# Kernel tuning notes

Hardware: AMD Instinct MI355X
Metric: run time of the kernel (lower is better)

## Reference

```python
import jax, jax.numpy as jnp
import numpy as np

B, TQ, TK, H = 8, 64, 8192, 256


def setup_inputs() -> dict:
    key = jax.random.key(0)
    k1, k2, k3, k4 = jax.random.split(key, 4)
    query = jax.random.normal(k1, (B, TQ, H), dtype=jnp.float32)
    keys = jax.random.normal(k2, (B, TK, H), dtype=jnp.float32)
    # nn.Linear(H, H): weight [H, H], bias [H]; scale like torch default-ish
    Wa_w = jax.random.normal(k3, (H, H), dtype=jnp.float32) * (1.0 / np.sqrt(H))
    Wa_b = jax.random.normal(k4, (H,), dtype=jnp.float32) * 0.01
    return {"query": query, "keys": keys, "Wa_w": Wa_w, "Wa_b": Wa_b}


def reference(query, keys, Wa_w, Wa_b):
    # keys_transformed = keys @ Wa_w.T + Wa_b  (torch Linear semantics)
    keys_t = jnp.einsum('bkh,oh->bko', keys, Wa_w) + Wa_b  # [B,TK,H]
    scores = jnp.einsum('bqh,bkh->bqk', query, keys_t)       # [B,TQ,TK]
    weights = jax.nn.softmax(scores, axis=-1)
    context = jnp.einsum('bqk,bkh->bqh', weights, keys)      # [B,TQ,H]
    return (context, weights)
```

## Files before the change

kernel.cpp:

```cpp
#include <hip/hip_runtime.h>

#define B 8
#define TQ 64
#define TK 8192
#define H 256

#define SPADB 72

#define KSPLIT 32
#define KPB (TK / KSPLIT)
#define CH 64
#define CKC 64
#define CPAD 68

typedef __attribute__((ext_vector_type(8))) short bf16x8;
typedef __attribute__((ext_vector_type(4))) float f32x4;
typedef __attribute__((ext_vector_type(4))) unsigned short u16x4;

static __device__ inline unsigned short f2bf(float x) {
    unsigned int u = __float_as_uint(x);
    unsigned int r = (u + 0x7fffu + ((u >> 16) & 1u)) >> 16;
    return (unsigned short)r;
}
static __device__ inline float bf2f(unsigned short h) {
    return __uint_as_float(((unsigned int)h) << 16);
}

__global__ __launch_bounds__(256) void qtransform_kernel(
    const float* __restrict__ query, const float* __restrict__ Wa_w,
    const float* __restrict__ Wa_b, float* __restrict__ qt, float* __restrict__ qb)
{
    __shared__ float q_s[H];
    __shared__ float red[4];
    const int r = blockIdx.x;
    const int t = threadIdx.x;
    q_s[t] = query[r * H + t];
    __syncthreads();

    float a0 = 0.f, a1 = 0.f, a2 = 0.f, a3 = 0.f;
    for (int o = 0; o < H; o += 4) {
        a0 += q_s[o + 0] * Wa_w[(o + 0) * H + t];
        a1 += q_s[o + 1] * Wa_w[(o + 1) * H + t];
        a2 += q_s[o + 2] * Wa_w[(o + 2) * H + t];
        a3 += q_s[o + 3] * Wa_w[(o + 3) * H + t];
    }
    qt[r * H + t] = (a0 + a1) + (a2 + a3);

    float p = q_s[t] * Wa_b[t];
    for (int off = 32; off > 0; off >>= 1) p += __shfl_down(p, off, 64);
    if ((t & 63) == 0) red[t >> 6] = p;
    __syncthreads();
    if (t == 0) qb[r] = (red[0] + red[1]) + (red[2] + red[3]);
}

__global__ __launch_bounds__(256) void scores_kernel(
    const float* __restrict__ qt, const float* __restrict__ qb,
    const float* __restrict__ keys, float* __restrict__ wout)
{
    __shared__ unsigned short a_hi[TQ][SPADB], a_lo[TQ][SPADB];
    __shared__ unsigned short b_hi[64][SPADB], b_lo[64][SPADB];
    const int t    = threadIdx.x;
    const int kt   = blockIdx.x;
    const int b    = blockIdx.y;
    const int k0g  = kt * 64;
    const int w    = t >> 6;
    const int lane = t & 63;
    const int lrow = lane & 15;
    const int lgrp = lane >> 4;

    f32x4 acc[4];
    #pragma unroll
    for (int nt = 0; nt < 4; ++nt) acc[nt] = (f32x4){0.f, 0.f, 0.f, 0.f};

    for (int hc = 0; hc < H; hc += 64) {
        __syncthreads();
        #pragma unroll
        for (int i = 0; i < 4; ++i) {
            int idx = t + 256 * i;
            int row = idx >> 4, hf = idx & 15;
            float4 va = *(const float4*)&qt[(b * TQ + row) * H + hc + hf * 4];
            u16x4 h4, l4;
            h4[0] = f2bf(va.x); l4[0] = f2bf(va.x - bf2f(h4[0]));
            h4[1] = f2bf(va.y); l4[1] = f2bf(va.y - bf2f(h4[1]));
            h4[2] = f2bf(va.z); l4[2] = f2bf(va.z - bf2f(h4[2]));
            h4[3] = f2bf(va.w); l4[3] = f2bf(va.w - bf2f(h4[3]));
            *(u16x4*)&a_hi[row][hf * 4] = h4;
            *(u16x4*)&a_lo[row][hf * 4] = l4;

            float4 vb = *(const float4*)&keys[(size_t)(b * TK + k0g + row) * H + hc + hf * 4];
            u16x4 g4, m4;
            g4[0] = f2bf(vb.x); m4[0] = f2bf(vb.x - bf2f(g4[0]));
            g4[1] = f2bf(vb.y); m4[1] = f2bf(vb.y - bf2f(g4[1]));
            g4[2] = f2bf(vb.z); m4[2] = f2bf(vb.z - bf2f(g4[2]));
            g4[3] = f2bf(vb.w); m4[3] = f2bf(vb.w - bf2f(g4[3]));
            *(u16x4*)&b_hi[row][hf * 4] = g4;
            *(u16x4*)&b_lo[row][hf * 4] = m4;
        }
        __syncthreads();
        #pragma unroll
        for (int hs = 0; hs < 64; hs += 32) {
            bf16x8 ah = *(const bf16x8*)&a_hi[16 * w + lrow][hs + lgrp * 8];
            bf16x8 al = *(const bf16x8*)&a_lo[16 * w + lrow][hs + lgrp * 8];
            #pragma unroll
            for (int nt = 0; nt < 4; ++nt) {
                bf16x8 bh = *(const bf16x8*)&b_hi[16 * nt + lrow][hs + lgrp * 8];
                bf16x8 bl = *(const bf16x8*)&b_lo[16 * nt + lrow][hs + lgrp * 8];
                acc[nt] = __builtin_amdgcn_mfma_f32_16x16x32_bf16(ah, bh, acc[nt], 0, 0, 0);
                acc[nt] = __builtin_amdgcn_mfma_f32_16x16x32_bf16(ah, bl, acc[nt], 0, 0, 0);
                acc[nt] = __builtin_amdgcn_mfma_f32_16x16x32_bf16(al, bh, acc[nt], 0, 0, 0);
            }
        }
    }
    #pragma unroll
    for (int j = 0; j < 4; ++j) {
        const int qrow = 16 * w + lgrp * 4 + j;
        const float bias = qb[b * TQ + qrow];
        float* dst = &wout[(size_t)(b * TQ + qrow) * TK + k0g + lrow];
        #pragma unroll
        for (int nt = 0; nt < 4; ++nt) dst[16 * nt] = acc[nt][j] + bias;
    }
}

__global__ __launch_bounds__(1024) void softmax_kernel(float* __restrict__ w)
{
    const int r = blockIdx.x;
    const int t = threadIdx.x;
    float4* row4 = (float4*)(w + (size_t)r * TK);
    __shared__ float redm[16];
    __shared__ float reds[16];
    const int wid = t >> 6, lane = t & 63;

    float4 v0 = row4[t];
    float4 v1 = row4[t + 1024];
    float m = fmaxf(fmaxf(fmaxf(v0.x, v0.y), fmaxf(v0.z, v0.w)),
                    fmaxf(fmaxf(v1.x, v1.y), fmaxf(v1.z, v1.w)));
    for (int off = 32; off > 0; off >>= 1) m = fmaxf(m, __shfl_xor(m, off, 64));
    if (lane == 0) redm[wid] = m;
    __syncthreads();
    m = redm[0];
    #pragma unroll
    for (int i = 1; i < 16; ++i) m = fmaxf(m, redm[i]);

    v0.x = __expf(v0.x - m); v0.y = __expf(v0.y - m);
    v0.z = __expf(v0.z - m); v0.w = __expf(v0.w - m);
    v1.x = __expf(v1.x - m); v1.y = __expf(v1.y - m);
    v1.z = __expf(v1.z - m); v1.w = __expf(v1.w - m);
    float s = (v0.x + v0.y + v0.z + v0.w) + (v1.x + v1.y + v1.z + v1.w);
    for (int off = 32; off > 0; off >>= 1) s += __shfl_xor(s, off, 64);
    if (lane == 0) reds[wid] = s;
    __syncthreads();
    s = reds[0];
    #pragma unroll
    for (int i = 1; i < 16; ++i) s += reds[i];
    const float inv = 1.0f / s;

    v0.x *= inv; v0.y *= inv; v0.z *= inv; v0.w *= inv;
    v1.x *= inv; v1.y *= inv; v1.z *= inv; v1.w *= inv;
    row4[t] = v0;
    row4[t + 1024] = v1;
}

__global__ __launch_bounds__(256) void context_main_kernel(
    const float* __restrict__ w, const float* __restrict__ keys,
    float* __restrict__ part)
{
    __shared__ float w_s[TQ][CPAD];
    __shared__ float k_s[CKC][CPAD];
    const int t  = threadIdx.x;
    const int ks = blockIdx.x;
    const int ht = blockIdx.y;
    const int b  = blockIdx.z;
    const int tq = t >> 4, th = t & 15;
    const int q0 = tq * 4, h0 = th * 4;

    float acc[4][4];
    #pragma unroll
    for (int i = 0; i < 4; ++i)
        #pragma unroll
        for (int j = 0; j < 4; ++j) acc[i][j] = 0.f;

    for (int kc = 0; kc < KPB; kc += CKC) {
        const int k0 = ks * KPB + kc;
        __syncthreads();
        #pragma unroll
        for (int i = 0; i < 4; ++i) {
            int idx = t + 256 * i;
            int q = idx >> 4, kf = idx & 15;
            *(float4*)&w_s[q][kf * 4] =
                *(const float4*)&w[(size_t)(b * TQ + q) * TK + k0 + kf * 4];
        }
        #pragma unroll
        for (int i = 0; i < 4; ++i) {
            int idx = t + 256 * i;
            int k = idx >> 4, hf = idx & 15;
            *(float4*)&k_s[k][hf * 4] =
                *(const float4*)&keys[(size_t)(b * TK + k0 + k) * H + ht * CH + hf * 4];
        }
        __syncthreads();
        #pragma unroll 4
        for (int k = 0; k < CKC; k += 4) {
            float4 wv[4], kv[4];
            #pragma unroll
            for (int i = 0; i < 4; ++i) wv[i] = *(const float4*)&w_s[q0 + i][k];
            #pragma unroll
            for (int j = 0; j < 4; ++j) kv[j] = *(const float4*)&k_s[k + j][h0];
            #pragma unroll
            for (int i = 0; i < 4; ++i) {
                acc[i][0] += wv[i].x * kv[0].x + wv[i].y * kv[1].x + wv[i].z * kv[2].x + wv[i].w * kv[3].x;
                acc[i][1] += wv[i].x * kv[0].y + wv[i].y * kv[1].y + wv[i].z * kv[2].y + wv[i].w * kv[3].y;
                acc[i][2] += wv[i].x * kv[0].z + wv[i].y * kv[1].z + wv[i].z * kv[2].z + wv[i].w * kv[3].z;
                acc[i][3] += wv[i].x * kv[0].w + wv[i].y * kv[1].w + wv[i].z * kv[2].w + wv[i].w * kv[3].w;
            }
        }
    }
    float* dst = part + (size_t)ks * (B * TQ * H);
    #pragma unroll
    for (int i = 0; i < 4; ++i) {
        float4 o = make_float4(acc[i][0], acc[i][1], acc[i][2], acc[i][3]);
        *(float4*)&dst[(size_t)(b * TQ + q0 + i) * H + ht * CH + h0] = o;
    }
}

__global__ __launch_bounds__(256) void context_reduce_kernel(
    const float* __restrict__ part, float* __restrict__ ctx)
{
    const int idx = blockIdx.x * 256 + threadIdx.x;
    float4 s = make_float4(0.f, 0.f, 0.f, 0.f);
    #pragma unroll 8
    for (int ks = 0; ks < KSPLIT; ++ks) {
        float4 v = *(const float4*)&part[(size_t)ks * (B * TQ * H) + (size_t)idx * 4];
        s.x += v.x; s.y += v.y; s.z += v.z; s.w += v.w;
    }
    *(float4*)&ctx[(size_t)idx * 4] = s;
}

extern "C" void kernel_launch(void* const* d_in, const int* in_sizes, int n_in,
                              void* d_out, int out_size, void* d_ws, size_t ws_size,
                              hipStream_t stream) {
    const float* query = (const float*)d_in[0];
    const float* keys  = (const float*)d_in[1];
    const float* Wa_w  = (const float*)d_in[2];
    const float* Wa_b  = (const float*)d_in[3];

    float* ctx = (float*)d_out;
    float* wts = (float*)d_out + B * TQ * H;
    float* qt  = (float*)d_ws;
    float* qb  = qt + B * TQ * H;
    float* part = qb + 512;

    qtransform_kernel<<<B * TQ, 256, 0, stream>>>(query, Wa_w, Wa_b, qt, qb);
    scores_kernel<<<dim3(TK / 64, B), 256, 0, stream>>>(qt, qb, keys, wts);
    softmax_kernel<<<B * TQ, 1024, 0, stream>>>(wts);
    context_main_kernel<<<dim3(KSPLIT, H / CH, B), 256, 0, stream>>>(wts, keys, part);
    context_reduce_kernel<<<(B * TQ * H / 4) / 256, 256, 0, stream>>>(part, ctx);
}
```

Before: 175.2 us.

## Run context GEMM on bf16 MFMA using precomputed bf16 keys and probabilities

The scores kernel now also writes a truncated bf16 copy of keys to workspace, and the softmax writes a bf16 copy of the probabilities. The context GEMM then reads these halved-size operands and uses MFMA 16x16x32 bf16 with a swizzled transposed LDS tile, replacing scalar fp32 FMAs. The split of query into bf16 hi/lo parts moves into qtransform, and key splitting switches to truncation instead of round-to-nearest. The risks are lower accuracy in the context output, since it uses a single bf16 term per operand, and extra global writes for the bf16 copies.

New measurement: 158.9 us. 9.3% less time.

```diff
diff --git a/kernel.cpp b/kernel.cpp
--- a/kernel.cpp
+++ b/kernel.cpp
@@ -9,26 +9,23 @@
 
 #define KSPLIT 32
 #define KPB (TK / KSPLIT)
-#define CH 64
-#define CKC 64
-#define CPAD 68
+#define CRS 72
 
 typedef __attribute__((ext_vector_type(8))) short bf16x8;
 typedef __attribute__((ext_vector_type(4))) float f32x4;
 typedef __attribute__((ext_vector_type(4))) unsigned short u16x4;
-
-static __device__ inline unsigned short f2bf(float x) {
+typedef __attribute__((ext_vector_type(2))) unsigned int u32x2;
+
+static __device__ inline unsigned short f2bf_rne(float x) {
     unsigned int u = __float_as_uint(x);
     unsigned int r = (u + 0x7fffu + ((u >> 16) & 1u)) >> 16;
     return (unsigned short)r;
 }
-static __device__ inline float bf2f(unsigned short h) {
-    return __uint_as_float(((unsigned int)h) << 16);
-}
 
 __global__ __launch_bounds__(256) void qtransform_kernel(
     const float* __restrict__ query, const float* __restrict__ Wa_w,
-    const float* __restrict__ Wa_b, float* __restrict__ qt, float* __restrict__ qb)
+    const float* __restrict__ Wa_b, unsigned short* __restrict__ qthi,
+    unsigned short* __restrict__ qtlo, float* __restrict__ qb)
 {
     __shared__ float q_s[H];
     __shared__ float red[4];
@@ -44,7 +41,12 @@
         a2 += q_s[o + 2] * Wa_w[(o + 2) * H + t];
         a3 += q_s[o + 3] * Wa_w[(o + 3) * H + t];
     }
-    qt[r * H + t] = (a0 + a1) + (a2 + a3);
+    const float s = (a0 + a1) + (a2 + a3);
+    const unsigned int u = __float_as_uint(s);
+    const float hif = __uint_as_float(u & 0xFFFF0000u);
+    const float lof = s - hif;
+    qthi[r * H + t] = (unsigned short)(u >> 16);
+    qtlo[r * H + t] = (unsigned short)(__float_as_uint(lof) >> 16);
 
     float p = q_s[t] * Wa_b[t];
     for (int off = 32; off > 0; off >>= 1) p += __shfl_down(p, off, 64);
@@ -54,8 +56,9 @@
 }
 
 __global__ __launch_bounds__(256) void scores_kernel(
-    const float* __restrict__ qt, const float* __restrict__ qb,
-    const float* __restrict__ keys, float* __restrict__ wout)
+    const unsigned short* __restrict__ qthi, const unsigned short* __restrict__ qtlo,
+    const float* __restrict__ qb, const float* __restrict__ keys,
+    unsigned short* __restrict__ khi_ws, float* __restrict__ wout)
 {
     __shared__ unsigned short a_hi[TQ][SPADB], a_lo[TQ][SPADB];
     __shared__ unsigned short b_hi[64][SPADB], b_lo[64][SPADB];
@@ -78,23 +81,29 @@
         for (int i = 0; i < 4; ++i) {
             int idx = t + 256 * i;
             int row = idx >> 4, hf = idx & 15;
-            float4 va = *(const float4*)&qt[(b * TQ + row) * H + hc + hf * 4];
-            u16x4 h4, l4;
-            h4[0] = f2bf(va.x); l4[0] = f2bf(va.x - bf2f(h4[0]));
-            h4[1] = f2bf(va.y); l4[1] = f2bf(va.y - bf2f(h4[1]));
-            h4[2] = f2bf(va.z); l4[2] = f2bf(va.z - bf2f(h4[2]));
-            h4[3] = f2bf(va.w); l4[3] = f2bf(va.w - bf2f(h4[3]));
-            *(u16x4*)&a_hi[row][hf * 4] = h4;
-            *(u16x4*)&a_lo[row][hf * 4] = l4;
-
+            *(u16x4*)&a_hi[row][hf * 4] =
+                *(const u16x4*)&qthi[(b * TQ + row) * H + hc + hf * 4];
+            *(u16x4*)&a_lo[row][hf * 4] =
+                *(const u16x4*)&qtlo[(b * TQ + row) * H + hc + hf * 4];
+        }
+        #pragma unroll
+        for (int i = 0; i < 4; ++i) {
+            int idx = t + 256 * i;
+            int row = idx >> 4, hf = idx & 15;
             float4 vb = *(const float4*)&keys[(size_t)(b * TK + k0g + row) * H + hc + hf * 4];
-            u16x4 g4, m4;
-            g4[0] = f2bf(vb.x); m4[0] = f2bf(vb.x - bf2f(g4[0]));
-            g4[1] = f2bf(vb.y); m4[1] = f2bf(vb.y - bf2f(g4[1]));
-            g4[2] = f2bf(vb.z); m4[2] = f2bf(vb.z - bf2f(g4[2]));
-            g4[3] = f2bf(vb.w); m4[3] = f2bf(vb.w - bf2f(g4[3]));
-            *(u16x4*)&b_hi[row][hf * 4] = g4;
-            *(u16x4*)&b_lo[row][hf * 4] = m4;
+            unsigned int u0 = __float_as_uint(vb.x), u1 = __float_as_uint(vb.y);
+            unsigned int u2 = __float_as_uint(vb.z), u3 = __float_as_uint(vb.w);
+            unsigned int h01 = (u0 >> 16) | (u1 & 0xFFFF0000u);
+            unsigned int h23 = (u2 >> 16) | (u3 & 0xFFFF0000u);
+            float l0 = vb.x - __uint_as_float(u0 & 0xFFFF0000u);
+            float l1 = vb.y - __uint_as_float(u1 & 0xFFFF0000u);
+            float l2 = vb.z - __uint_as_float(u2 & 0xFFFF0000u);
+            float l3 = vb.w - __uint_as_float(u3 & 0xFFFF0000u);
+            unsigned int l01 = (__float_as_uint(l0) >> 16) | (__float_as_uint(l1) & 0xFFFF0000u);
+            unsigned int l23 = (__float_as_uint(l2) >> 16) | (__float_as_uint(l3) & 0xFFFF0000u);
+            *(u32x2*)&b_hi[row][hf * 4] = (u32x2){h01, h23};
+            *(u32x2*)&b_lo[row][hf * 4] = (u32x2){l01, l23};
+            *(u32x2*)&khi_ws[((size_t)b * TK + k0g + row) * H + hc + hf * 4] = (u32x2){h01, h23};
         }
         __syncthreads();
         #pragma unroll
@@ -121,7 +130,8 @@
     }
 }
 
-__global__ __launch_bounds__(1024) void softmax_kernel(float* __restrict__ w)
+__global__ __launch_bounds__(1024) void softmax_kernel(
+    float* __restrict__ w, unsigned short* __restrict__ phi)
 {
     const int r = blockIdx.x;
     const int t = threadIdx.x;
@@ -158,66 +168,70 @@
     v1.x *= inv; v1.y *= inv; v1.z *= inv; v1.w *= inv;
     row4[t] = v0;
     row4[t + 1024] = v1;
+
+    unsigned short* prow = phi + (size_t)r * TK;
+    u16x4 p0, p1;
+    p0[0] = f2bf_rne(v0.x); p0[1] = f2bf_rne(v0.y);
+    p0[2] = f2bf_rne(v0.z); p0[3] = f2bf_rne(v0.w);
+    p1[0] = f2bf_rne(v1.x); p1[1] = f2bf_rne(v1.y);
+    p1[2] = f2bf_rne(v1.z); p1[3] = f2bf_rne(v1.w);
+    *(u16x4*)&prow[t * 4] = p0;
+    *(u16x4*)&prow[4096 + t * 4] = p1;
 }
 
 __global__ __launch_bounds__(256) void context_main_kernel(
-    const float* __restrict__ w, const float* __restrict__ keys,
+    const unsigned short* __restrict__ phi, const unsigned short* __restrict__ khi,
     float* __restrict__ part)
 {
-    __shared__ float w_s[TQ][CPAD];
-    __shared__ float k_s[CKC][CPAD];
-    const int t  = threadIdx.x;
-    const int ks = blockIdx.x;
-    const int ht = blockIdx.y;
-    const int b  = blockIdx.z;
-    const int tq = t >> 4, th = t & 15;
-    const int q0 = tq * 4, h0 = th * 4;
-
-    float acc[4][4];
-    #pragma unroll
-    for (int i = 0; i < 4; ++i)
-        #pragma unroll
-        for (int j = 0; j < 4; ++j) acc[i][j] = 0.f;
-
-    for (int kc = 0; kc < KPB; kc += CKC) {
-        const int k0 = ks * KPB + kc;
+    __shared__ unsigned short kT[64 * CRS];
+    const int t    = threadIdx.x;
+    const int ks   = blockIdx.x;
+    const int ht   = blockIdx.y;
+    const int b    = blockIdx.z;
+    const int w    = t >> 6;
+    const int lane = t & 63;
+    const int lrow = lane & 15;
+    const int lgrp = lane >> 4;
+
+    f32x4 acc[4];
+    #pragma unroll
+    for (int nt = 0; nt < 4; ++nt) acc[nt] = (f32x4){0.f, 0.f, 0.f, 0.f};
+
+    const int kbase = ks * KPB;
+    for (int c = 0; c < KPB; c += 64) {
         __syncthreads();
         #pragma unroll
         for (int i = 0; i < 4; ++i) {
             int idx = t + 256 * i;
-            int q = idx >> 4, kf = idx & 15;
-            *(float4*)&w_s[q][kf * 4] =
-                *(const float4*)&w[(size_t)(b * TQ + q) * TK + k0 + kf * 4];
-        }
-        #pragma unroll
-        for (int i = 0; i < 4; ++i) {
-            int idx = t + 256 * i;
-            int k = idx >> 4, hf = idx & 15;
-            *(float4*)&k_s[k][hf * 4] =
-                *(const float4*)&keys[(size_t)(b * TK + k0 + k) * H + ht * CH + hf * 4];
-        }
-        __syncthreads();
-        #pragma unroll 4
-        for (int k = 0; k < CKC; k += 4) {
-            float4 wv[4], kv[4];
+            int k = idx >> 4, hq = idx & 15;
+            u16x4 v = *(const u16x4*)&khi[((size_t)b * TK + kbase + c + k) * H + ht * 64 + hq * 4];
             #pragma unroll
-            for (int i = 0; i < 4; ++i) wv[i] = *(const float4*)&w_s[q0 + i][k];
+            for (int c4 = 0; c4 < 4; ++c4) {
+                int h = hq * 4 + c4;
+                kT[h * CRS + (((k >> 3) ^ ((h >> 3) & 7)) << 3) + (k & 7)] = v[c4];
+            }
+        }
+        __syncthreads();
+        #pragma unroll
+        for (int kc = 0; kc < 64; kc += 32) {
+            bf16x8 af = *(const bf16x8*)&phi[((size_t)(b * TQ) + 16 * w + lrow) * TK
+                                             + kbase + c + kc + lgrp * 8];
             #pragma unroll
-            for (int j = 0; j < 4; ++j) kv[j] = *(const float4*)&k_s[k + j][h0];
-            #pragma unroll
-            for (int i = 0; i < 4; ++i) {
-                acc[i][0] += wv[i].x * kv[0].x + wv[i].y * kv[1].x + wv[i].z * kv[2].x + wv[i].w * kv[3].x;
-                acc[i][1] += wv[i].x * kv[0].y + wv[i].y * kv[1].y + wv[i].z * kv[2].y + wv[i].w * kv[3].y;
-                acc[i][2] += wv[i].x * kv[0].z + wv[i].y * kv[1].z + wv[i].z * kv[2].z + wv[i].w * kv[3].z;
-                acc[i][3] += wv[i].x * kv[0].w + wv[i].y * kv[1].w + wv[i].z * kv[2].w + wv[i].w * kv[3].w;
+            for (int nt = 0; nt < 4; ++nt) {
+                int h = 16 * nt + lrow;
+                bf16x8 bf = *(const bf16x8*)&kT[h * CRS
+                              + ((((kc >> 3) + lgrp) ^ ((h >> 3) & 7)) << 3)];
+                acc[nt] = __builtin_amdgcn_mfma_f32_16x16x32_bf16(af, bf, acc[nt], 0, 0, 0);
             }
         }
     }
     float* dst = part + (size_t)ks * (B * TQ * H);
     #pragma unroll
-    for (int i = 0; i < 4; ++i) {
-        float4 o = make_float4(acc[i][0], acc[i][1], acc[i][2], acc[i][3]);
-        *(float4*)&dst[(size_t)(b * TQ + q0 + i) * H + ht * CH + h0] = o;
+    for (int j = 0; j < 4; ++j) {
+        const int qrow = 16 * w + lgrp * 4 + j;
+        #pragma unroll
+        for (int nt = 0; nt < 4; ++nt)
+            dst[(size_t)(b * TQ + qrow) * H + ht * 64 + 16 * nt + lrow] = acc[nt][j];
     }
 }
 
@@ -244,13 +258,18 @@
 
     float* ctx = (float*)d_out;
     float* wts = (float*)d_out + B * TQ * H;
-    float* qt  = (float*)d_ws;
-    float* qb  = qt + B * TQ * H;
-    float* part = qb + 512;
-
-    qtransform_kernel<<<B * TQ, 256, 0, stream>>>(query, Wa_w, Wa_b, qt, qb);
-    scores_kernel<<<dim3(TK / 64, B), 256, 0, stream>>>(qt, qb, keys, wts);
-    softmax_kernel<<<B * TQ, 1024, 0, stream>>>(wts);
-    context_main_kernel<<<dim3(KSPLIT, H / CH, B), 256, 0, stream>>>(wts, keys, part);
+
+    char* p = (char*)d_ws;
+    float* part = (float*)p;            p += (size_t)KSPLIT * B * TQ * H * 4;
+    unsigned short* khi = (unsigned short*)p;  p += (size_t)B * TK * H * 2;
+    unsigned short* phi = (unsigned short*)p;  p += (size_t)B * TQ * TK * 2;
+    unsigned short* qthi = (unsigned short*)p; p += (size_t)B * TQ * H * 2;
+    unsigned short* qtlo = (unsigned short*)p; p += (size_t)B * TQ * H * 2;
+    float* qb = (float*)p;
+
+    qtransform_kernel<<<B * TQ, 256, 0, stream>>>(query, Wa_w, Wa_b, qthi, qtlo, qb);
+    scores_kernel<<<dim3(TK / 64, B), 256, 0, stream>>>(qthi, qtlo, qb, keys, khi, wts);
+    softmax_kernel<<<B * TQ, 1024, 0, stream>>>(wts, phi);
+    context_main_kernel<<<dim3(KSPLIT, 4, B), 256, 0, stream>>>(phi, khi, part);
     context_reduce_kernel<<<(B * TQ * H / 4) / 256, 256, 0, stream>>>(part, ctx);
 }
```
